# Optimization experiments

Hardware: AMD Instinct MI355X
Metric: run time of the kernel (lower is better)

## Reference

```python
import jax, jax.numpy as jnp
import numpy as np

D_MODEL = 1024
NUM_HEADS = 16
D_K = D_MODEL // NUM_HEADS
WINDOW = 256


def setup_inputs() -> dict:
    key = jax.random.key(0)
    ks = jax.random.split(key, 11)
    B, S, D = 2, 2048, D_MODEL
    scale = 1.0 / np.sqrt(D)
    inp = {
        "q": jax.random.normal(ks[0], (B, S, D), jnp.float32),
        "k": jax.random.normal(ks[1], (B, S, D), jnp.float32),
        "v": jax.random.normal(ks[2], (B, S, D), jnp.float32),
        "Wq": jax.random.normal(ks[3], (D, D), jnp.float32) * scale,
        "bq": jnp.zeros((D,), jnp.float32),
        "Wk": jax.random.normal(ks[4], (D, D), jnp.float32) * scale,
        "bk": jnp.zeros((D,), jnp.float32),
        "Wv": jax.random.normal(ks[5], (D, D), jnp.float32) * scale,
        "bv": jnp.zeros((D,), jnp.float32),
        "Wo": jax.random.normal(ks[6], (D, D), jnp.float32) * scale,
        "bo": jnp.zeros((D,), jnp.float32),
    }
    return inp


def _split_heads(x):
    B, S, _ = x.shape
    return x.reshape(B, S, NUM_HEADS, D_K).transpose(0, 2, 1, 3)  # [B,H,S,d_k]


def reference(q, k, v, Wq, bq, Wk, bk, Wv, bv, Wo, bo):
    B, S, D = q.shape
    qh = _split_heads(q @ Wq + bq)
    kh = _split_heads(k @ Wk + bk)
    vh = _split_heads(v @ Wv + bv)

    # dense scores then sliding-window band mask (|i-j| <= WINDOW), as in SparseAttention
    scores = jnp.einsum("bhqd,bhkd->bhqk", qh, kh) / jnp.sqrt(jnp.float32(D_K))
    idx = jnp.arange(S)
    band = jnp.abs(idx[:, None] - idx[None, :]) <= WINDOW  # [S,S]
    scores = jnp.where(band[None, None], scores, -jnp.inf)
    attn = jax.nn.softmax(scores, axis=-1)

    out = jnp.einsum("bhqk,bhkd->bhqd", attn, vh)
    out = out.transpose(0, 2, 1, 3).reshape(B, S, D)  # combine heads
    out = out @ Wo + bo
    return out, attn
```

## Files before the change

### kernel.cpp

```cpp
#include <hip/hip_runtime.h>


constexpr int Bb = 2, Ss = 2048, Dd = 1024, Hh = 16, WINw = 256;
constexpr size_t XS_SLAB = (size_t)4096 * 2048;
constexpr size_t WT_SLAB = (size_t)1024 * 2048;
constexpr size_t QB_SLAB = (size_t)4096 * 1024;

typedef short s16x8 __attribute__((ext_vector_type(8)));
typedef float f32x4 __attribute__((ext_vector_type(4)));

typedef __attribute__((address_space(3))) unsigned int lds_uint;
typedef const __attribute__((address_space(1))) unsigned int gbl_uint;

__device__ __forceinline__ void gld_lds16(const void* g, void* l) {
  __builtin_amdgcn_global_load_lds((gbl_uint*)g, (lds_uint*)l, 16, 0, 0);
}

__device__ inline unsigned short f2bf(float x) {
  unsigned u = __float_as_uint(x);
  u += 0x7fff + ((u >> 16) & 1);
  return (unsigned short)(u >> 16);
}
__device__ inline float bf2f(unsigned short h) {
  return __uint_as_float(((unsigned)h) << 16);
}

__global__ __launch_bounds__(256) void convert_x(
    const float* __restrict__ x0, const float* __restrict__ x1,
    const float* __restrict__ x2, unsigned short* __restrict__ Xs) {
  int z = blockIdx.z;
  const float* src = z == 0 ? x0 : (z == 1 ? x1 : x2);
  unsigned short* dst = Xs + (size_t)z * XS_SLAB;
  size_t idx = ((size_t)blockIdx.x * 256 + threadIdx.x) * 4;
  int r = (int)(idx >> 10);
  int c = (int)(idx & 1023);
  f32x4 v = *(const f32x4*)&src[idx];
  unsigned short hi[4], lo[4];
#pragma unroll
  for (int i = 0; i < 4; ++i) {
    float vi = v[i];
    hi[i] = f2bf(vi);
    lo[i] = f2bf(vi - bf2f(hi[i]));
  }
  ushort4 h4 = {hi[0], hi[1], hi[2], hi[3]};
  ushort4 l4 = {lo[0], lo[1], lo[2], lo[3]};
  *(ushort4*)&dst[(size_t)r * 2048 + c] = h4;
  *(ushort4*)&dst[(size_t)r * 2048 + 1024 + c] = l4;
}

__global__ __launch_bounds__(256) void convert_w(
    const float* __restrict__ w0, const float* __restrict__ w1,
    const float* __restrict__ w2, const float* __restrict__ w3,
    unsigned short* __restrict__ Wt) {
  __shared__ float T[64][65];
  int z = blockIdx.z;
  const float* W = z == 0 ? w0 : (z == 1 ? w1 : (z == 2 ? w2 : w3));
  unsigned short* dst = Wt + (size_t)z * WT_SLAB;
  int k0 = blockIdx.y * 64, n0 = blockIdx.x * 64;
  int t = threadIdx.x;
#pragma unroll
  for (int i = 0; i < 4; ++i) {
    int row = (t >> 4) + i * 16;
    int c4 = (t & 15) * 4;
    f32x4 v = *(const f32x4*)&W[(size_t)(k0 + row) * 1024 + n0 + c4];
    T[row][c4 + 0] = v[0]; T[row][c4 + 1] = v[1];
    T[row][c4 + 2] = v[2]; T[row][c4 + 3] = v[3];
  }
  __syncthreads();
  int n = t >> 2;
  int kc = (t & 3) * 16;
  unsigned short hi[16], lo[16];
#pragma unroll
  for (int j = 0; j < 16; ++j) {
    float x = T[kc + j][n];
    hi[j] = f2bf(x);
    lo[j] = f2bf(x - bf2f(hi[j]));
  }
  size_t base = (size_t)(n0 + n) * 2048 + k0 + kc;
#pragma unroll
  for (int j4 = 0; j4 < 4; ++j4) {
    ushort4 h4 = {hi[j4 * 4], hi[j4 * 4 + 1], hi[j4 * 4 + 2], hi[j4 * 4 + 3]};
    ushort4 l4 = {lo[j4 * 4], lo[j4 * 4 + 1], lo[j4 * 4 + 2], lo[j4 * 4 + 3]};
    *(ushort4*)&dst[base + j4 * 4] = h4;
    *(ushort4*)&dst[base + 1024 + j4 * 4] = l4;
  }
}

template <int F32OUT>
__global__ __launch_bounds__(256, 3) void gemm_bf16x3(
    const unsigned short* __restrict__ Abase,
    const unsigned short* __restrict__ Wtbase, void* __restrict__ Cbase,
    const float* __restrict__ bb0, const float* __restrict__ bb1,
    const float* __restrict__ bb2) {
  __shared__ s16x8 As[2][512];
  __shared__ s16x8 Bs[2][512];
  int z = blockIdx.z;
  const unsigned short* A = Abase + (size_t)z * XS_SLAB;
  const unsigned short* Wt = Wtbase + (size_t)z * WT_SLAB;
  const float* bias = z == 0 ? bb0 : (z == 1 ? bb1 : bb2);
  const float scl = (!F32OUT && z == 0) ? 0.125f : 1.0f;

  const int t = threadIdx.x;
  const int lane = t & 63, wave = t >> 6;
  const int wm = wave & 1, wn = wave >> 1;
  const int bm = blockIdx.y * 128, bn = blockIdx.x * 128;

  f32x4 acc[4][4] = {};

  const int s0 = t, s1 = t + 256;
  const int r0 = s0 >> 2, c0 = (s0 & 3) ^ ((r0 >> 1) & 3);
  const int r1 = s1 >> 2, c1 = (s1 & 3) ^ ((r1 >> 1) & 3);
  const unsigned short* A0 = A + (size_t)(bm + r0) * 2048 + c0 * 8;
  const unsigned short* A1 = A + (size_t)(bm + r1) * 2048 + c1 * 8;
  const unsigned short* B0 = Wt + (size_t)(bn + r0) * 2048 + c0 * 8;
  const unsigned short* B1 = Wt + (size_t)(bn + r1) * 2048 + c1 * 8;

  const int m15 = lane & 15, q = lane >> 4;

  gld_lds16(A0, &As[0][wave * 64]);
  gld_lds16(A1, &As[0][256 + wave * 64]);
  gld_lds16(B0, &Bs[0][wave * 64]);
  gld_lds16(B1, &Bs[0][256 + wave * 64]);
  __syncthreads();

  int cur = 0;
  for (int kb = 0; kb < 3072; kb += 32) {
    const int kn = kb + 32;
    if (kn < 3072) {
      int asrc = kn < 1024 ? kn : kn - 1024;
      int wsrc = kn < 2048 ? kn : kn - 2048;
      gld_lds16(A0 + asrc, &As[cur ^ 1][wave * 64]);
      gld_lds16(A1 + asrc, &As[cur ^ 1][256 + wave * 64]);
      gld_lds16(B0 + wsrc, &Bs[cur ^ 1][wave * 64]);
      gld_lds16(B1 + wsrc, &Bs[cur ^ 1][256 + wave * 64]);
    }

    s16x8 af[4], bf[4];
#pragma unroll
    for (int mt = 0; mt < 4; ++mt) {
      int r = wm * 64 + mt * 16 + m15;
      af[mt] = As[cur][r * 4 + (q ^ ((r >> 1) & 3))];
    }
#pragma unroll
    for (int nt = 0; nt < 4; ++nt) {
      int r = wn * 64 + nt * 16 + m15;
      bf[nt] = Bs[cur][r * 4 + (q ^ ((r >> 1) & 3))];
    }
#pragma unroll
    for (int mt = 0; mt < 4; ++mt)
#pragma unroll
      for (int nt = 0; nt < 4; ++nt)
        acc[mt][nt] = __builtin_amdgcn_mfma_f32_16x16x32_bf16(
            af[mt], bf[nt], acc[mt][nt], 0, 0, 0);

    if (kn < 3072) {
      __syncthreads();
      cur ^= 1;
    }
  }

#pragma unroll
  for (int nt = 0; nt < 4; ++nt) {
    int col = bn + wn * 64 + nt * 16 + m15;
    float bv = bias[col];
#pragma unroll
    for (int mt = 0; mt < 4; ++mt) {
      int rowb = bm + wm * 64 + mt * 16 + q * 4;
#pragma unroll
      for (int i = 0; i < 4; ++i) {
        float val = (acc[mt][nt][i] + bv) * scl;
        if (F32OUT) {
          __builtin_nontemporal_store(
              val, &((float*)Cbase)[(size_t)(rowb + i) * 1024 + col]);
        } else {
          ((unsigned short*)Cbase + (size_t)z * QB_SLAB)
              [(size_t)(rowb + i) * 1024 + col] = f2bf(val);
        }
      }
    }
  }
}

__global__ __launch_bounds__(256) void transpose_v(
    const unsigned short* __restrict__ Vb, unsigned short* __restrict__ Vt) {
  __shared__ unsigned short T[64][88];
  const int b = blockIdx.z, h = blockIdx.y, s0 = blockIdx.x * 64;
  const int t = threadIdx.x;
  {
    int row = t >> 2, part = t & 3;
    const unsigned short* src =
        Vb + (size_t)(b * Ss + s0 + row) * 1024 + h * 64 + part * 16;
    s16x8 v0 = *(const s16x8*)src;
    s16x8 v1 = *(const s16x8*)(src + 8);
    *(s16x8*)&T[row][part * 16] = v0;
    *(s16x8*)&T[row][part * 16 + 8] = v1;
  }
  __syncthreads();
  {
    int d = t & 63, sw = t >> 6;
    unsigned short tmp[16];
#pragma unroll
    for (int i = 0; i < 16; ++i) tmp[i] = T[sw * 16 + i][d];
    unsigned short* dst =
        Vt + ((size_t)((b * Hh + h) * 64 + d)) * 2048 + s0 + sw * 16;
    *(s16x8*)dst = *(const s16x8*)&tmp[0];
    *(s16x8*)(dst + 8) = *(const s16x8*)&tmp[8];
  }
}

constexpr int SW3 = 556;
__global__ __launch_bounds__(256) void attn_v3(
    const unsigned short* __restrict__ Qb, const unsigned short* __restrict__ Kb,
    const unsigned short* __restrict__ Vt, float* __restrict__ attn,
    unsigned short* __restrict__ XsAO) {
  __shared__ float P[16 * SW3];
  const int t = threadIdx.x;
  const int lane = t & 63, wave = t >> 6;
  const int m15 = lane & 15, quad = lane >> 4;
  const int bid = blockIdx.x;
  const int qt = bid & 127, h = (bid >> 7) & 15, b = bid >> 11;
  const int q0 = qt * 16;
  int jlo = q0 - WINw; if (jlo < 0) jlo = 0;
  int jhi = q0 + 15 + WINw; if (jhi > Ss - 1) jhi = Ss - 1;
  const int ncols = jhi - jlo + 1;
  const int ntiles = ncols >> 4;

  {
    const unsigned short* qrow =
        Qb + (size_t)(b * Ss + q0 + m15) * 1024 + h * 64 + quad * 8;
    s16x8 aq0 = *(const s16x8*)qrow;
    s16x8 aq1 = *(const s16x8*)(qrow + 32);
    for (int nt = wave; nt < ntiles; nt += 4) {
      const unsigned short* krow =
          Kb + (size_t)(b * Ss + jlo + nt * 16 + m15) * 1024 + h * 64 + quad * 8;
      s16x8 b0 = *(const s16x8*)krow;
      s16x8 b1 = *(const s16x8*)(krow + 32);
      f32x4 c = {0.f, 0.f, 0.f, 0.f};
      c = __builtin_amdgcn_mfma_f32_16x16x32_bf16(aq0, b0, c, 0, 0, 0);
      c = __builtin_amdgcn_mfma_f32_16x16x32_bf16(aq1, b1, c, 0, 0, 0);
      float* pp = &P[(quad * 4) * SW3 + nt * 16 + m15];
#pragma unroll
      for (int i = 0; i < 4; ++i) pp[i * SW3] = c[i];
    }
  }
  __syncthreads();

  {
#pragma unroll
    for (int ri = 0; ri < 4; ++ri) {
      const int r = wave * 4 + ri;
      const int qq = q0 + r;
      int lo = qq - WINw; if (lo < 0) lo = 0;
      int hi = qq + WINw; if (hi > Ss - 1) hi = Ss - 1;
      const int clo = lo - jlo, chi = hi - jlo;
      float sv[9];
      bool ib[9];
      float m = -1e30f;
#pragma unroll
      for (int k2 = 0; k2 < 9; ++k2) {
        int c = k2 * 64 + lane;
        bool inb = (c >= clo) && (c <= chi);
        ib[k2] = inb;
        float vv = inb ? P[r * SW3 + c] : -1e30f;
        sv[k2] = vv;
        m = fmaxf(m, vv);
      }
#pragma unroll
      for (int off = 32; off; off >>= 1) m = fmaxf(m, __shfl_xor(m, off, 64));
      float e[9], l = 0.f;
#pragma unroll
      for (int k2 = 0; k2 < 9; ++k2) { e[k2] = __expf(sv[k2] - m); l += e[k2]; }
#pragma unroll
      for (int off = 32; off; off >>= 1) l += __shfl_xor(l, off, 64);
      const float inv = 1.f / l;
#pragma unroll
      for (int k2 = 0; k2 < 9; ++k2) {
        int c = k2 * 64 + lane;
        if (c < 544) P[r * SW3 + c] = ib[k2] ? e[k2] * inv : 0.f;
      }
      float* arow = attn + ((size_t)((b * Hh + h) * Ss + qq)) * Ss;
#pragma unroll
      for (int i = 0; i < 8; ++i) {
        int col = i * 256 + lane * 4;
        int c = col - jlo;
        f32x4 v = {0.f, 0.f, 0.f, 0.f};
        if (c >= 0 && c <= 540) v = *(const f32x4*)&P[r * SW3 + c];
        __builtin_nontemporal_store(v, (f32x4*)&arow[col]);
      }
    }
  }
  __syncthreads();

  {
    const int ntk = (ncols + 31) >> 5;
    const unsigned short* vtrow =
        Vt + ((size_t)((b * Hh + h) * 64 + wave * 16 + m15)) * 2048 + jlo +
        quad * 8;
    f32x4 o = {0.f, 0.f, 0.f, 0.f};
    for (int ks = 0; ks < ntk; ++ks) {
      const float* pa = &P[m15 * SW3 + ks * 32 + quad * 8];
      f32x4 p0 = *(const f32x4*)pa;
      f32x4 p1 = *(const f32x4*)(pa + 4);
      s16x8 af;
#pragma unroll
      for (int i = 0; i < 4; ++i) af[i] = (short)f2bf(p0[i]);
#pragma unroll
      for (int i = 0; i < 4; ++i) af[4 + i] = (short)f2bf(p1[i]);
      s16x8 bf = *(const s16x8*)(vtrow + ks * 32);
      o = __builtin_amdgcn_mfma_f32_16x16x32_bf16(af, bf, o, 0, 0, 0);
    }
    const int dcol = h * 64 + wave * 16 + m15;
#pragma unroll
    for (int i = 0; i < 4; ++i) {
      int row = q0 + quad * 4 + i;
      unsigned short hi = f2bf(o[i]);
      unsigned short lo = f2bf(o[i] - bf2f(hi));
      unsigned short* dst = XsAO + (size_t)(b * Ss + row) * 2048 + dcol;
      dst[0] = hi;
      dst[1024] = lo;
    }
  }
}

extern "C" void kernel_launch(void* const* d_in, const int* in_sizes, int n_in,
                              void* d_out, int out_size, void* d_ws,
                              size_t ws_size, hipStream_t stream) {
  const float* q  = (const float*)d_in[0];
  const float* k  = (const float*)d_in[1];
  const float* v  = (const float*)d_in[2];
  const float* Wq = (const float*)d_in[3];
  const float* bq = (const float*)d_in[4];
  const float* Wk = (const float*)d_in[5];
  const float* bk = (const float*)d_in[6];
  const float* Wv = (const float*)d_in[7];
  const float* bv = (const float*)d_in[8];
  const float* Wo = (const float*)d_in[9];
  const float* bo = (const float*)d_in[10];

  float* out = (float*)d_out;
  float* attn = out + (size_t)Bb * Ss * Dd;

  unsigned short* Xs   = (unsigned short*)d_ws;
  unsigned short* XsAO = Xs + 3 * XS_SLAB;
  unsigned short* Wt   = XsAO + XS_SLAB;
  unsigned short* Qb   = Wt + 4 * WT_SLAB;
  unsigned short* Kb   = Qb + QB_SLAB;
  unsigned short* Vb   = Kb + QB_SLAB;
  unsigned short* Vt   = Vb + QB_SLAB;

  hipLaunchKernelGGL(convert_x, dim3(4096, 1, 3), dim3(256), 0, stream,
                     q, k, v, Xs);
  hipLaunchKernelGGL(convert_w, dim3(16, 16, 4), dim3(256), 0, stream,
                     Wq, Wk, Wv, Wo, Wt);
  hipLaunchKernelGGL((gemm_bf16x3<0>), dim3(8, 32, 3), dim3(256), 0, stream,
                     Xs, Wt, (void*)Qb, bq, bk, bv);
  hipLaunchKernelGGL(transpose_v, dim3(32, 16, 2), dim3(256), 0, stream,
                     Vb, Vt);
  hipLaunchKernelGGL(attn_v3, dim3(Bb * Hh * (Ss / 16)), dim3(256), 0, stream,
                     Qb, Kb, Vt, attn, XsAO);
  hipLaunchKernelGGL((gemm_bf16x3<1>), dim3(8, 32, 1), dim3(256), 0, stream,
                     XsAO, Wt + 3 * WT_SLAB, (void*)out, bo, bo, bo);
}
```

Baseline: 787.0 us.

## Merge convert kernels, retile output GEMM, add MFMA priority and lighter barriers

Folds the x and weight conversion kernels into one launch that dispatches on block id, removing one kernel launch. Splits the output projection into a dedicated GEMM with 64x128 tiles, doubling the grid from 256 to 512 blocks so more CUs are busy on the single-slab output GEMM. In attention, wraps the MFMA calls in s_setprio and replaces __syncthreads with an explicit lgkmcnt wait plus s_barrier. The smaller tile reloads the weight tile more often per output element and lowers MFMA reuse per LDS load.

```diff
diff --git a/kernel.cpp b/kernel.cpp
--- a/kernel.cpp
+++ b/kernel.cpp
@@ -16,6 +16,11 @@
   __builtin_amdgcn_global_load_lds((gbl_uint*)g, (lds_uint*)l, 16, 0, 0);
 }
 
+__device__ __forceinline__ void lgkm_barrier() {
+  asm volatile("s_waitcnt lgkmcnt(0)" ::: "memory");
+  __builtin_amdgcn_s_barrier();
+}
+
 __device__ inline unsigned short f2bf(float x) {
   unsigned u = __float_as_uint(x);
   u += 0x7fff + ((u >> 16) & 1);
@@ -25,80 +30,84 @@
   return __uint_as_float(((unsigned)h) << 16);
 }
 
-__global__ __launch_bounds__(256) void convert_x(
+__global__ __launch_bounds__(256) void convert_xw(
     const float* __restrict__ x0, const float* __restrict__ x1,
-    const float* __restrict__ x2, unsigned short* __restrict__ Xs) {
-  int z = blockIdx.z;
-  const float* src = z == 0 ? x0 : (z == 1 ? x1 : x2);
-  unsigned short* dst = Xs + (size_t)z * XS_SLAB;
-  size_t idx = ((size_t)blockIdx.x * 256 + threadIdx.x) * 4;
-  int r = (int)(idx >> 10);
-  int c = (int)(idx & 1023);
-  f32x4 v = *(const f32x4*)&src[idx];
-  unsigned short hi[4], lo[4];
-#pragma unroll
-  for (int i = 0; i < 4; ++i) {
-    float vi = v[i];
-    hi[i] = f2bf(vi);
-    lo[i] = f2bf(vi - bf2f(hi[i]));
-  }
-  ushort4 h4 = {hi[0], hi[1], hi[2], hi[3]};
-  ushort4 l4 = {lo[0], lo[1], lo[2], lo[3]};
-  *(ushort4*)&dst[(size_t)r * 2048 + c] = h4;
-  *(ushort4*)&dst[(size_t)r * 2048 + 1024 + c] = l4;
-}
-
-__global__ __launch_bounds__(256) void convert_w(
+    const float* __restrict__ x2, unsigned short* __restrict__ Xs,
     const float* __restrict__ w0, const float* __restrict__ w1,
     const float* __restrict__ w2, const float* __restrict__ w3,
     unsigned short* __restrict__ Wt) {
   __shared__ float T[64][65];
-  int z = blockIdx.z;
-  const float* W = z == 0 ? w0 : (z == 1 ? w1 : (z == 2 ? w2 : w3));
-  unsigned short* dst = Wt + (size_t)z * WT_SLAB;
-  int k0 = blockIdx.y * 64, n0 = blockIdx.x * 64;
-  int t = threadIdx.x;
-#pragma unroll
-  for (int i = 0; i < 4; ++i) {
-    int row = (t >> 4) + i * 16;
-    int c4 = (t & 15) * 4;
-    f32x4 v = *(const f32x4*)&W[(size_t)(k0 + row) * 1024 + n0 + c4];
-    T[row][c4 + 0] = v[0]; T[row][c4 + 1] = v[1];
-    T[row][c4 + 2] = v[2]; T[row][c4 + 3] = v[3];
-  }
-  __syncthreads();
-  int n = t >> 2;
-  int kc = (t & 3) * 16;
-  unsigned short hi[16], lo[16];
-#pragma unroll
-  for (int j = 0; j < 16; ++j) {
-    float x = T[kc + j][n];
-    hi[j] = f2bf(x);
-    lo[j] = f2bf(x - bf2f(hi[j]));
-  }
-  size_t base = (size_t)(n0 + n) * 2048 + k0 + kc;
-#pragma unroll
-  for (int j4 = 0; j4 < 4; ++j4) {
-    ushort4 h4 = {hi[j4 * 4], hi[j4 * 4 + 1], hi[j4 * 4 + 2], hi[j4 * 4 + 3]};
-    ushort4 l4 = {lo[j4 * 4], lo[j4 * 4 + 1], lo[j4 * 4 + 2], lo[j4 * 4 + 3]};
-    *(ushort4*)&dst[base + j4 * 4] = h4;
-    *(ushort4*)&dst[base + 1024 + j4 * 4] = l4;
-  }
-}
-
-template <int F32OUT>
-__global__ __launch_bounds__(256, 3) void gemm_bf16x3(
+  const int id = blockIdx.x;
+  const int t = threadIdx.x;
+  if (id < 12288) {
+    int z = id >> 12;
+    int bx = id & 4095;
+    const float* src = z == 0 ? x0 : (z == 1 ? x1 : x2);
+    unsigned short* dst = Xs + (size_t)z * XS_SLAB;
+    size_t idx = ((size_t)bx * 256 + t) * 4;
+    int r = (int)(idx >> 10);
+    int c = (int)(idx & 1023);
+    f32x4 v = *(const f32x4*)&src[idx];
+    unsigned short hi[4], lo[4];
+#pragma unroll
+    for (int i = 0; i < 4; ++i) {
+      float vi = v[i];
+      hi[i] = f2bf(vi);
+      lo[i] = f2bf(vi - bf2f(hi[i]));
+    }
+    ushort4 h4 = {hi[0], hi[1], hi[2], hi[3]};
+    ushort4 l4 = {lo[0], lo[1], lo[2], lo[3]};
+    *(ushort4*)&dst[(size_t)r * 2048 + c] = h4;
+    *(ushort4*)&dst[(size_t)r * 2048 + 1024 + c] = l4;
+  } else {
+    int wid = id - 12288;
+    int z = wid >> 8;
+    int by = (wid >> 4) & 15;
+    int bx = wid & 15;
+    const float* W = z == 0 ? w0 : (z == 1 ? w1 : (z == 2 ? w2 : w3));
+    unsigned short* dst = Wt + (size_t)z * WT_SLAB;
+    int k0 = by * 64, n0 = bx * 64;
+#pragma unroll
+    for (int i = 0; i < 4; ++i) {
+      int row = (t >> 4) + i * 16;
+      int c4 = (t & 15) * 4;
+      f32x4 v = *(const f32x4*)&W[(size_t)(k0 + row) * 1024 + n0 + c4];
+      T[row][c4 + 0] = v[0]; T[row][c4 + 1] = v[1];
+      T[row][c4 + 2] = v[2]; T[row][c4 + 3] = v[3];
+    }
+    __syncthreads();
+    int n = t >> 2;
+    int kc = (t & 3) * 16;
+    unsigned short hi[16], lo[16];
+#pragma unroll
+    for (int j = 0; j < 16; ++j) {
+      float x = T[kc + j][n];
+      hi[j] = f2bf(x);
+      lo[j] = f2bf(x - bf2f(hi[j]));
+    }
+    size_t base = (size_t)(n0 + n) * 2048 + k0 + kc;
+#pragma unroll
+    for (int j4 = 0; j4 < 4; ++j4) {
+      ushort4 h4 = {hi[j4 * 4], hi[j4 * 4 + 1], hi[j4 * 4 + 2], hi[j4 * 4 + 3]};
+      ushort4 l4 = {lo[j4 * 4], lo[j4 * 4 + 1], lo[j4 * 4 + 2], lo[j4 * 4 + 3]};
+      *(ushort4*)&dst[base + j4 * 4] = h4;
+      *(ushort4*)&dst[base + 1024 + j4 * 4] = l4;
+    }
+  }
+}
+
+__global__ __launch_bounds__(256, 3) void gemm_qkv(
     const unsigned short* __restrict__ Abase,
-    const unsigned short* __restrict__ Wtbase, void* __restrict__ Cbase,
-    const float* __restrict__ bb0, const float* __restrict__ bb1,
-    const float* __restrict__ bb2) {
+    const unsigned short* __restrict__ Wtbase,
+    unsigned short* __restrict__ Cbase, const float* __restrict__ bb0,
+    const float* __restrict__ bb1, const float* __restrict__ bb2) {
   __shared__ s16x8 As[2][512];
   __shared__ s16x8 Bs[2][512];
   int z = blockIdx.z;
   const unsigned short* A = Abase + (size_t)z * XS_SLAB;
   const unsigned short* Wt = Wtbase + (size_t)z * WT_SLAB;
   const float* bias = z == 0 ? bb0 : (z == 1 ? bb1 : bb2);
-  const float scl = (!F32OUT && z == 0) ? 0.125f : 1.0f;
+  const float scl = (z == 0) ? 0.125f : 1.0f;
 
   const int t = threadIdx.x;
   const int lane = t & 63, wave = t >> 6;
@@ -169,13 +178,87 @@
 #pragma unroll
       for (int i = 0; i < 4; ++i) {
         float val = (acc[mt][nt][i] + bv) * scl;
-        if (F32OUT) {
-          __builtin_nontemporal_store(
-              val, &((float*)Cbase)[(size_t)(rowb + i) * 1024 + col]);
-        } else {
-          ((unsigned short*)Cbase + (size_t)z * QB_SLAB)
-              [(size_t)(rowb + i) * 1024 + col] = f2bf(val);
-        }
+        (Cbase + (size_t)z * QB_SLAB)[(size_t)(rowb + i) * 1024 + col] =
+            f2bf(val);
+      }
+    }
+  }
+}
+
+__global__ __launch_bounds__(256, 2) void gemm_out(
+    const unsigned short* __restrict__ A,
+    const unsigned short* __restrict__ Wt,
+    float* __restrict__ C, const float* __restrict__ bias) {
+  __shared__ s16x8 As[2][256];
+  __shared__ s16x8 Bs[2][512];
+  const int t = threadIdx.x;
+  const int lane = t & 63, wave = t >> 6;
+  const int wm = wave & 1, wn = wave >> 1;
+  const int bm = blockIdx.y * 64, bn = blockIdx.x * 128;
+
+  f32x4 acc[2][4] = {};
+
+  const int ra = t >> 2, ca = (t & 3) ^ ((ra >> 1) & 3);
+  const int s0 = t, s1 = t + 256;
+  const int r0 = s0 >> 2, c0 = (s0 & 3) ^ ((r0 >> 1) & 3);
+  const int r1 = s1 >> 2, c1 = (s1 & 3) ^ ((r1 >> 1) & 3);
+  const unsigned short* Ap = A + (size_t)(bm + ra) * 2048 + ca * 8;
+  const unsigned short* B0 = Wt + (size_t)(bn + r0) * 2048 + c0 * 8;
+  const unsigned short* B1 = Wt + (size_t)(bn + r1) * 2048 + c1 * 8;
+
+  const int m15 = lane & 15, q = lane >> 4;
+
+  gld_lds16(Ap, &As[0][wave * 64]);
+  gld_lds16(B0, &Bs[0][wave * 64]);
+  gld_lds16(B1, &Bs[0][256 + wave * 64]);
+  __syncthreads();
+
+  int cur = 0;
+  for (int kb = 0; kb < 3072; kb += 32) {
+    const int kn = kb + 32;
+    if (kn < 3072) {
+      int asrc = kn < 1024 ? kn : kn - 1024;
+      int wsrc = kn < 2048 ? kn : kn - 2048;
+      gld_lds16(Ap + asrc, &As[cur ^ 1][wave * 64]);
+      gld_lds16(B0 + wsrc, &Bs[cur ^ 1][wave * 64]);
+      gld_lds16(B1 + wsrc, &Bs[cur ^ 1][256 + wave * 64]);
+    }
+
+    s16x8 af[2], bf[4];
+#pragma unroll
+    for (int mt = 0; mt < 2; ++mt) {
+      int r = wm * 32 + mt * 16 + m15;
+      af[mt] = As[cur][r * 4 + (q ^ ((r >> 1) & 3))];
+    }
+#pragma unroll
+    for (int nt = 0; nt < 4; ++nt) {
+      int r = wn * 64 + nt * 16 + m15;
+      bf[nt] = Bs[cur][r * 4 + (q ^ ((r >> 1) & 3))];
+    }
+#pragma unroll
+    for (int mt = 0; mt < 2; ++mt)
+#pragma unroll
+      for (int nt = 0; nt < 4; ++nt)
+        acc[mt][nt] = __builtin_amdgcn_mfma_f32_16x16x32_bf16(
+            af[mt], bf[nt], acc[mt][nt], 0, 0, 0);
+
+    if (kn < 3072) {
+      __syncthreads();
+      cur ^= 1;
+    }
+  }
+
+#pragma unroll
+  for (int nt = 0; nt < 4; ++nt) {
+    int col = bn + wn * 64 + nt * 16 + m15;
+    float bv = bias[col];
+#pragma unroll
+    for (int mt = 0; mt < 2; ++mt) {
+      int rowb = bm + wm * 32 + mt * 16 + q * 4;
+#pragma unroll
+      for (int i = 0; i < 4; ++i) {
+        __builtin_nontemporal_store(
+            acc[mt][nt][i] + bv, &C[(size_t)(rowb + i) * 1024 + col]);
       }
     }
   }
@@ -209,7 +292,7 @@
 }
 
 constexpr int SW3 = 556;
-__global__ __launch_bounds__(256) void attn_v3(
+__global__ __launch_bounds__(256) void attn_v4(
     const unsigned short* __restrict__ Qb, const unsigned short* __restrict__ Kb,
     const unsigned short* __restrict__ Vt, float* __restrict__ attn,
     unsigned short* __restrict__ XsAO) {
@@ -236,14 +319,16 @@
       s16x8 b0 = *(const s16x8*)krow;
       s16x8 b1 = *(const s16x8*)(krow + 32);
       f32x4 c = {0.f, 0.f, 0.f, 0.f};
+      __builtin_amdgcn_s_setprio(1);
       c = __builtin_amdgcn_mfma_f32_16x16x32_bf16(aq0, b0, c, 0, 0, 0);
       c = __builtin_amdgcn_mfma_f32_16x16x32_bf16(aq1, b1, c, 0, 0, 0);
+      __builtin_amdgcn_s_setprio(0);
       float* pp = &P[(quad * 4) * SW3 + nt * 16 + m15];
 #pragma unroll
       for (int i = 0; i < 4; ++i) pp[i * SW3] = c[i];
     }
   }
-  __syncthreads();
+  lgkm_barrier();
 
   {
 #pragma unroll
@@ -289,7 +374,7 @@
       }
     }
   }
-  __syncthreads();
+  lgkm_barrier();
 
   {
     const int ntk = (ncols + 31) >> 5;
@@ -307,7 +392,9 @@
 #pragma unroll
       for (int i = 0; i < 4; ++i) af[4 + i] = (short)f2bf(p1[i]);
       s16x8 bf = *(const s16x8*)(vtrow + ks * 32);
+      __builtin_amdgcn_s_setprio(1);
       o = __builtin_amdgcn_mfma_f32_16x16x32_bf16(af, bf, o, 0, 0, 0);
+      __builtin_amdgcn_s_setprio(0);
     }
     const int dcol = h * 64 + wave * 16 + m15;
 #pragma unroll
@@ -348,16 +435,14 @@
   unsigned short* Vb   = Kb + QB_SLAB;
   unsigned short* Vt   = Vb + QB_SLAB;
 
-  hipLaunchKernelGGL(convert_x, dim3(4096, 1, 3), dim3(256), 0, stream,
-                     q, k, v, Xs);
-  hipLaunchKernelGGL(convert_w, dim3(16, 16, 4), dim3(256), 0, stream,
-                     Wq, Wk, Wv, Wo, Wt);
-  hipLaunchKernelGGL((gemm_bf16x3<0>), dim3(8, 32, 3), dim3(256), 0, stream,
-                     Xs, Wt, (void*)Qb, bq, bk, bv);
+  hipLaunchKernelGGL(convert_xw, dim3(12288 + 1024), dim3(256), 0, stream,
+                     q, k, v, Xs, Wq, Wk, Wv, Wo, Wt);
+  hipLaunchKernelGGL(gemm_qkv, dim3(8, 32, 3), dim3(256), 0, stream,
+                     Xs, Wt, Qb, bq, bk, bv);
   hipLaunchKernelGGL(transpose_v, dim3(32, 16, 2), dim3(256), 0, stream,
                      Vb, Vt);
-  hipLaunchKernelGGL(attn_v3, dim3(Bb * Hh * (Ss / 16)), dim3(256), 0, stream,
+  hipLaunchKernelGGL(attn_v4, dim3(Bb * Hh * (Ss / 16)), dim3(256), 0, stream,
                      Qb, Kb, Vt, attn, XsAO);
-  hipLaunchKernelGGL((gemm_bf16x3<1>), dim3(8, 32, 1), dim3(256), 0, stream,
-                     XsAO, Wt + 3 * WT_SLAB, (void*)out, bo, bo, bo);
-}
+  hipLaunchKernelGGL(gemm_out, dim3(8, 64, 1), dim3(256), 0, stream,
+                     XsAO, Wt + 3 * WT_SLAB, out, bo);
+}
```

Result: no change. 784.1 us (-0.4%).
